# Kernel optimization log

Hardware: AMD Instinct MI355X
Metric: run time of the kernel (lower is better)

## Reference

```python
import jax, jax.numpy as jnp
import numpy as np

N_NODES = 50000
N_EDGES = 1000000
N_EVAL = 100000
IN_DIM = 256
HID = 64
HEADS = 4
NEG_SLOPE = 0.2


def _glorot(key, shape):
    fan_in, fan_out = shape[0], shape[-1]
    lim = jnp.sqrt(6.0 / (fan_in + fan_out))
    return jax.random.uniform(key, shape, jnp.float32, -lim, lim)


def setup_inputs() -> dict:
    key = jax.random.key(0)
    ks = jax.random.split(key, 24)
    inp = {}
    inp["x"] = jax.random.normal(ks[0], (N_NODES, IN_DIM), jnp.float32)
    inp["edge_index"] = jax.random.randint(ks[1], (2, N_EDGES), 0, N_NODES, jnp.int64)
    inp["edge_src"] = jax.random.randint(ks[2], (N_EVAL,), 0, N_NODES, jnp.int64)
    inp["edge_dst"] = jax.random.randint(ks[3], (N_EVAL,), 0, N_NODES, jnp.int64)
    # encoder
    inp["enc_w"] = _glorot(ks[4], (IN_DIM, HID))
    inp["enc_b"] = jnp.zeros((HID,), jnp.float32)
    # GAT layer 1: HID -> HEADS*HID (concat)
    inp["gat1_w"] = _glorot(ks[5], (HID, HEADS * HID))
    inp["gat1_att_src"] = _glorot(ks[6], (HEADS, HID))
    inp["gat1_att_dst"] = _glorot(ks[7], (HEADS, HID))
    inp["gat1_b"] = jnp.zeros((HEADS * HID,), jnp.float32)
    # GAT layer 2: HEADS*HID -> HEADS*HID
    inp["gat2_w"] = _glorot(ks[8], (HEADS * HID, HEADS * HID))
    inp["gat2_att_src"] = _glorot(ks[9], (HEADS, HID))
    inp["gat2_att_dst"] = _glorot(ks[10], (HEADS, HID))
    inp["gat2_b"] = jnp.zeros((HEADS * HID,), jnp.float32)
    # link predictor MLP: 2*256 -> 64 -> 32 -> 1
    inp["lp1_w"] = _glorot(ks[11], (2 * HEADS * HID, HID))
    inp["lp1_b"] = jnp.zeros((HID,), jnp.float32)
    inp["lp2_w"] = _glorot(ks[12], (HID, HID // 2))
    inp["lp2_b"] = jnp.zeros((HID // 2,), jnp.float32)
    inp["lp3_w"] = _glorot(ks[13], (HID // 2, 1))
    inp["lp3_b"] = jnp.zeros((1,), jnp.float32)
    return inp


def gat_layer(x, src, dst, W, att_src, att_dst, bias, n_nodes):
    # x: [N, F_in] -> h: [N, H, C]
    h = (x @ W).reshape(n_nodes, HEADS, HID)
    a_s = jnp.einsum("nhc,hc->nh", h, att_src)  # per-node src logit part
    a_d = jnp.einsum("nhc,hc->nh", h, att_dst)  # per-node dst logit part
    e = jax.nn.leaky_relu(a_s[src] + a_d[dst], NEG_SLOPE)  # [E, H]
    # segment softmax over incoming edges of each dst node
    m = jax.ops.segment_max(e, dst, num_segments=n_nodes)  # [N, H]
    e = jnp.exp(e - m[dst])
    s = jax.ops.segment_sum(e, dst, num_segments=n_nodes)  # [N, H]
    alpha = e / (s[dst] + 1e-16)  # [E, H]
    msg = h[src] * alpha[:, :, None]  # [E, H, C]
    out = jax.ops.segment_sum(msg, dst, num_segments=n_nodes)  # [N, H, C]
    return out.reshape(n_nodes, HEADS * HID) + bias


def reference(x, edge_index, edge_src, edge_dst,
              enc_w, enc_b,
              gat1_w, gat1_att_src, gat1_att_dst, gat1_b,
              gat2_w, gat2_att_src, gat2_att_dst, gat2_b,
              lp1_w, lp1_b, lp2_w, lp2_b, lp3_w, lp3_b):
    n = x.shape[0]
    src, dst = edge_index[0], edge_index[1]
    # NodeEncoder
    h = jax.nn.relu(x @ enc_w + enc_b)
    # GAT layers (dropout is identity in eval)
    h = gat_layer(h, src, dst, gat1_w, gat1_att_src, gat1_att_dst, gat1_b, n)
    h = gat_layer(h, src, dst, gat2_w, gat2_att_src, gat2_att_dst, gat2_b, n)
    # link predictor on (src_feat, dst_feat) pairs
    pair = jnp.concatenate([h[edge_src], h[edge_dst]], axis=1)  # [Eval, 512]
    z = jax.nn.relu(pair @ lp1_w + lp1_b)
    z = jax.nn.relu(z @ lp2_w + lp2_b)
    scores = z @ lp3_w + lp3_b  # [Eval, 1]
    return scores
```

## Files before the change

kernel.cpp:

```cpp
#include <hip/hip_runtime.h>
#include <hip/hip_bf16.h>
#include <math.h>

#define NNODES 50000
#define HID    64
#define HEADS  4
#define FDIM   256

typedef __attribute__((ext_vector_type(8))) _Float16 half8v;
typedef __attribute__((ext_vector_type(4))) _Float16 half4v;
typedef __attribute__((ext_vector_type(4))) float f32x4;

__device__ __forceinline__ float lrelu(float x) { return fmaxf(x, 0.2f * x); }

__global__ void prep_kernel(const float4* __restrict__ x, _Float16* __restrict__ xh, int n4,
                            const float* __restrict__ enc_w, const float* __restrict__ g1_w,
                            const float* __restrict__ g2_w, const float* __restrict__ lp1_w,
                            const float* __restrict__ g1_as, const float* __restrict__ g1_ad,
                            const float* __restrict__ g2_as, const float* __restrict__ g2_ad,
                            _Float16* __restrict__ we, _Float16* __restrict__ w1,
                            _Float16* __restrict__ w2, _Float16* __restrict__ wlp)
{
  int t = blockIdx.x * blockDim.x + threadIdx.x;
  if (t < n4) {
    float4 v = x[t];
    half4v o = {(_Float16)v.x, (_Float16)v.y, (_Float16)v.z, (_Float16)v.w};
    *(half4v*)(xh + (size_t)t * 4) = o;
    return;
  }
  int u = t - n4;
  if (u < 16384) {
    int n = u >> 8, k = u & 255;
    we[u] = (_Float16)enc_w[(size_t)k * 64 + n];
  } else if (u < 32768) {
    int l = u - 16384; int n = l >> 6, k = l & 63;
    w1[l] = (_Float16)g1_w[(size_t)k * 256 + n];
  } else if (u < 98304) {
    int l = u - 32768; int n = l >> 8, k = l & 255;
    w2[l] = (_Float16)g2_w[(size_t)k * 256 + n];
  } else if (u < 131072) {
    int l = u - 98304; int n = l >> 8, k = l & 255;
    int srow = (n < 64) ? k : (256 + k);
    wlp[l] = (_Float16)lp1_w[(size_t)srow * 64 + (n & 63)];
  } else if (u < 132096) {
    int l = u - 131072; int j = l >> 6, k = l & 63;
    float v = 0.f;
    if (j < 8) {
      int head = j & 3;
      const float* att = (j < 4 ? g1_as : g1_ad) + head * 64;
      for (int c = 0; c < 64; ++c) v += g1_w[(size_t)k * 256 + head * 64 + c] * att[c];
    }
    w1[(256 + j) * 64 + k] = (_Float16)v;
  } else if (u < 136192) {
    int l = u - 132096; int j = l >> 8, k = l & 255;
    float v = 0.f;
    if (j < 8) {
      int head = j & 3;
      const float* att = (j < 4 ? g2_as : g2_ad) + head * 64;
      for (int c = 0; c < 64; ++c) v += g2_w[(size_t)k * 256 + head * 64 + c] * att[c];
    }
    w2[(256 + j) * 256 + k] = (_Float16)v;
  }
}

__global__ __launch_bounds__(256) void enc_gemm(
    const _Float16* __restrict__ A, const _Float16* __restrict__ B,
    const float* __restrict__ bias, _Float16* __restrict__ outH, int M)
{
  __shared__ _Float16 As[128 * 64];
  const int tid  = threadIdx.x;
  const int lane = tid & 63;
  const int wid  = tid >> 6;
  const int row0 = blockIdx.y * 128;

  f32x4 acc[2][4];
#pragma unroll
  for (int m = 0; m < 2; ++m)
#pragma unroll
    for (int n = 0; n < 4; ++n) acc[m][n] = (f32x4){0.f, 0.f, 0.f, 0.f};

  const int rsub = lane >> 3;
  const int slot = lane & 7;
  const int brow = lane & 15;
  const int bk   = (lane >> 4) * 8;

  for (int kt = 0; kt < 256; kt += 64) {
#pragma unroll
    for (int i = 0; i < 4; ++i) {
      const int c  = i * 4 + wid;
      const int r  = c * 8 + rsub;
      const int gr = min(row0 + r, M - 1);
      const int ss = slot ^ rsub;
      const size_t goff = (size_t)gr * 256 + kt + ss * 8;
      __builtin_amdgcn_global_load_lds(
          (const __attribute__((address_space(1))) void*)(A + goff),
          (__attribute__((address_space(3))) void*)(As + c * 512), 16, 0, 0);
    }
    __syncthreads();

#pragma unroll
    for (int ks = 0; ks < 2; ++ks) {
      half8v ah[2], bh[4];
#pragma unroll
      for (int mf = 0; mf < 2; ++mf) {
        const int r   = wid * 32 + mf * 16 + (lane & 15);
        const int sl  = (ks * 4 + (lane >> 4)) ^ (r & 7);
        ah[mf] = *(const half8v*)(As + r * 64 + sl * 8);
      }
#pragma unroll
      for (int nf = 0; nf < 4; ++nf)
        bh[nf] = *(const half8v*)(B + (size_t)(brow + nf * 16) * 256 + kt + ks * 32 + bk);
#pragma unroll
      for (int mf = 0; mf < 2; ++mf)
#pragma unroll
        for (int nf = 0; nf < 4; ++nf)
          acc[mf][nf] = __builtin_amdgcn_mfma_f32_16x16x32_f16(ah[mf], bh[nf], acc[mf][nf], 0, 0, 0);
    }
    __syncthreads();
  }

  const int crow = row0 + wid * 32 + (lane >> 4) * 4;
  const int ccol = lane & 15;
#pragma unroll
  for (int mf = 0; mf < 2; ++mf)
#pragma unroll
    for (int nf = 0; nf < 4; ++nf)
#pragma unroll
      for (int r = 0; r < 4; ++r) {
        const int grow = crow + mf * 16 + r;
        const int gcol = ccol + nf * 16;
        if (grow >= M) continue;
        float v = fmaxf(acc[mf][nf][r] + bias[gcol], 0.f);
        outH[(size_t)grow * HID + gcol] = (_Float16)v;
      }
}

template<int KTOT, bool LOGIT>
__global__ __launch_bounds__(512) void gemm512(
    const _Float16* __restrict__ A, const _Float16* __restrict__ B,
    _Float16* __restrict__ outH, float* __restrict__ a_s, float* __restrict__ a_d,
    int M, int OS)
{
  __shared__ _Float16 As[128 * KTOT];
  constexpr int SPR = KTOT / 8;
  const int tid  = threadIdx.x;
  const int lane = tid & 63;
  const int w    = tid >> 6;
  const int rowg = w & 3;
  const int colg = w >> 2;
  const int row0 = blockIdx.y * 128;
  const int col0 = blockIdx.x * 128 + colg * 64;
  const bool lastlog = LOGIT && ((int)blockIdx.x == (int)gridDim.x - 1) && (colg == 1);

#pragma unroll
  for (int rr = 0; rr < KTOT / 32; ++rr) {
    const int f  = rr * 512 + tid;
    const int r  = f / SPR;
    const int s  = f % SPR;
    const int gs = s ^ (r & 7);
    const int gr = min(row0 + r, M - 1);
    __builtin_amdgcn_global_load_lds(
        (const __attribute__((address_space(1))) void*)(A + (size_t)gr * KTOT + gs * 8),
        (__attribute__((address_space(3))) void*)(As + f * 8), 16, 0, 0);
  }
  __syncthreads();

  f32x4 acc[2][4];
  f32x4 accL[2];
#pragma unroll
  for (int m = 0; m < 2; ++m) {
#pragma unroll
    for (int n = 0; n < 4; ++n) acc[m][n] = (f32x4){0.f, 0.f, 0.f, 0.f};
    accL[m] = (f32x4){0.f, 0.f, 0.f, 0.f};
  }

  const int brow = col0 + (lane & 15);
#pragma unroll
  for (int ks = 0; ks < KTOT / 32; ++ks) {
    const int sk = ks * 4 + (lane >> 4);
    half8v ah[2];
#pragma unroll
    for (int mf = 0; mf < 2; ++mf) {
      const int r = rowg * 32 + mf * 16 + (lane & 15);
      ah[mf] = *(const half8v*)(As + r * KTOT + (sk ^ (r & 7)) * 8);
    }
#pragma unroll
    for (int nf = 0; nf < 4; ++nf) {
      const half8v bh = *(const half8v*)(B + (size_t)(brow + nf * 16) * KTOT + sk * 8);
      acc[0][nf] = __builtin_amdgcn_mfma_f32_16x16x32_f16(ah[0], bh, acc[0][nf], 0, 0, 0);
      acc[1][nf] = __builtin_amdgcn_mfma_f32_16x16x32_f16(ah[1], bh, acc[1][nf], 0, 0, 0);
    }
    if (lastlog) {
      const half8v bh = *(const half8v*)(B + (size_t)(256 + (lane & 15)) * KTOT + sk * 8);
      accL[0] = __builtin_amdgcn_mfma_f32_16x16x32_f16(ah[0], bh, accL[0], 0, 0, 0);
      accL[1] = __builtin_amdgcn_mfma_f32_16x16x32_f16(ah[1], bh, accL[1], 0, 0, 0);
    }
  }

  const int crow = row0 + rowg * 32 + (lane >> 4) * 4;
  const int ccol = col0 + (lane & 15);
#pragma unroll
  for (int mf = 0; mf < 2; ++mf)
#pragma unroll
    for (int nf = 0; nf < 4; ++nf)
#pragma unroll
      for (int r = 0; r < 4; ++r) {
        const int grow = crow + mf * 16 + r;
        if (grow >= M) continue;
        outH[(size_t)grow * OS + ccol + nf * 16] = (_Float16)acc[mf][nf][r];
      }
  if (lastlog) {
    const int c8 = lane & 15;
#pragma unroll
    for (int mf = 0; mf < 2; ++mf)
#pragma unroll
      for (int r = 0; r < 4; ++r) {
        const int grow = crow + mf * 16 + r;
        if (grow >= M) continue;
        const float v = accL[mf][r];
        if (c8 < 4)      a_s[grow * 4 + c8] = v;
        else if (c8 < 8) a_d[grow * 4 + (c8 - 4)] = v;
      }
  }
}

__global__ void hist_kernel(const int* __restrict__ dst, int* __restrict__ deg, int E)
{
  int i = blockIdx.x * blockDim.x + threadIdx.x;
  if (i < E) atomicAdd(&deg[dst[i]], 1);
}

__global__ void scan1_kernel(const int* __restrict__ deg, int* __restrict__ off,
                             int* __restrict__ bsum, int n)
{
  __shared__ int ws[4];
  const int t = threadIdx.x, lane = t & 63, w = t >> 6;
  const int i = blockIdx.x * 256 + t;
  const int v = (i < n) ? deg[i] : 0;
  int x = v;
#pragma unroll
  for (int d = 1; d < 64; d <<= 1) {
    int y = __shfl_up(x, d, 64);
    if (lane >= d) x += y;
  }
  if (lane == 63) ws[w] = x;
  __syncthreads();
  int add = 0;
  for (int k = 0; k < w; ++k) add += ws[k];
  if (i < n) off[i] = add + x - v;
  if (t == 255) bsum[blockIdx.x] = add + x;
}

__global__ void scan2_kernel(int* __restrict__ bsum, int nb)
{
  __shared__ int ws[4];
  const int t = threadIdx.x, lane = t & 63, w = t >> 6;
  const int v = (t < nb) ? bsum[t] : 0;
  int x = v;
#pragma unroll
  for (int d = 1; d < 64; d <<= 1) {
    int y = __shfl_up(x, d, 64);
    if (lane >= d) x += y;
  }
  if (lane == 63) ws[w] = x;
  __syncthreads();
  int add = 0;
  for (int k = 0; k < w; ++k) add += ws[k];
  if (t < nb) bsum[t] = add + x - v;
}

__global__ void scan3_kernel(int* __restrict__ off, const int* __restrict__ bsum, int n, int E)
{
  const int i = blockIdx.x * 256 + threadIdx.x;
  if (i < n) off[i] += bsum[blockIdx.x];
  if (i == 0) off[n] = E;
}

__global__ void scatter_kernel(const int* __restrict__ src, const int* __restrict__ dst,
                               const int* __restrict__ off, int* __restrict__ cursor,
                               int* __restrict__ sidx, int E)
{
  int i = blockIdx.x * blockDim.x + threadIdx.x;
  if (i < E) {
    int d = dst[i];
    int p = atomicAdd(&cursor[d], 1);
    sidx[off[d] + p] = src[i];
  }
}

__global__ __launch_bounds__(256) void aggregate_kernel(
    const _Float16* __restrict__ hW, const int* __restrict__ sidx,
    const int* __restrict__ off, const float* __restrict__ a_s, const float* __restrict__ a_d,
    const float* __restrict__ bias,
    _Float16* __restrict__ outH, int n_nodes)
{
  __shared__ float wlds[4][16][4];
  const int w    = threadIdx.x >> 6;
  const int wid  = (blockIdx.x * 256 + threadIdx.x) >> 6;
  const int lane = threadIdx.x & 63;
  if (wid >= n_nodes) return;
  const int n = wid;
  const int beg = off[n], end = off[n + 1];

  const int es   = lane >> 2;
  const int hh   = lane & 3;
  const float adh = a_d[(unsigned)n * 4 + hh];
  float m = -1e30f, ssum = 0.f;
  for (int j = beg + es; j < end; j += 16) {
    const unsigned s = (unsigned)sidx[j];
    const float e = lrelu(a_s[s * 4 + hh] + adh);
    const float mn = fmaxf(m, e);
    ssum = ssum * __expf(m - mn) + __expf(e - mn);
    m = mn;
  }
#pragma unroll
  for (int d = 4; d < 64; d <<= 1) {
    const float mo = __shfl_xor(m, d, 64);
    const float so = __shfl_xor(ssum, d, 64);
    const float mn = fmaxf(m, mo);
    ssum = ssum * __expf(m - mn) + so * __expf(mo - mn);
    m = mn;
  }
  const int hb = lane >> 4;
  const float sh = __shfl(ssum, hb, 64);

  float acc0 = 0.f, acc1 = 0.f, acc2 = 0.f, acc3 = 0.f;
  const unsigned lo4 = (unsigned)(lane << 2);
  for (int j0 = beg; j0 < end; j0 += 16) {
    const int jj = j0 + es;
    float wv = 0.f;
    if (jj < end) {
      const unsigned s = (unsigned)sidx[jj];
      const float e = lrelu(a_s[s * 4 + hh] + adh);
      wv = __expf(e - m);
    }
    wlds[w][es][hh] = wv;
    const int jend = min(j0 + 16, end);
#pragma unroll 4
    for (int j = j0; j < jend; ++j) {
      const unsigned s = (unsigned)sidx[j];
      const float wgt = wlds[w][j - j0][hb];
      const half4v hv = *(const half4v*)(hW + s * (unsigned)FDIM + lo4);
      acc0 = fmaf(wgt, (float)hv.x, acc0);
      acc1 = fmaf(wgt, (float)hv.y, acc1);
      acc2 = fmaf(wgt, (float)hv.z, acc2);
      acc3 = fmaf(wgt, (float)hv.w, acc3);
    }
  }
  const float inv = 1.f / (sh + 1e-16f);
  const float4 bv = *(const float4*)(bias + lo4);
  half4v o = {(_Float16)(acc0 * inv + bv.x), (_Float16)(acc1 * inv + bv.y),
              (_Float16)(acc2 * inv + bv.z), (_Float16)(acc3 * inv + bv.w)};
  *(half4v*)(outH + (unsigned)n * FDIM + lo4) = o;
}

__global__ __launch_bounds__(256) void linkpred_kernel(
    const _Float16* __restrict__ uv,
    const int* __restrict__ es, const int* __restrict__ ed,
    const float* __restrict__ b1, const float* __restrict__ w2, const float* __restrict__ b2,
    const float* __restrict__ w3, const float* __restrict__ b3,
    float* __restrict__ out, int n_eval)
{
  __shared__ float w2s[64 * 32];
  __shared__ float z1s[4][4][64];
  const int t = threadIdx.x;
  for (int i = t; i < 64 * 32; i += 256) w2s[i] = w2[i];
  const int w = t >> 6, lane = t & 63;
  const int pair0 = blockIdx.x * 16 + w * 4;
#pragma unroll
  for (int p = 0; p < 4; ++p) {
    const int pc = min(pair0 + p, n_eval - 1);
    const int s = es[pc], d = ed[pc];
    const float uvl = (float)uv[(unsigned)s * 128 + lane] + (float)uv[(unsigned)d * 128 + 64 + lane];
    z1s[w][p][lane] = fmaxf(uvl + b1[lane], 0.f);
  }
  __syncthreads();
  const int half = lane >> 5;
  const int col  = lane & 31;
  const float w3c = w3[col];
#pragma unroll
  for (int pp = 0; pp < 2; ++pp) {
    const int p = pp * 2 + half;
    float acc = b2[col];
#pragma unroll
    for (int k = 0; k < 64; ++k) acc = fmaf(z1s[w][p][k], w2s[k * 32 + col], acc);
    float zz = fmaxf(acc, 0.f) * w3c;
#pragma unroll
    for (int d = 1; d < 32; d <<= 1) zz += __shfl_xor(zz, d, 64);
    if (col == 0) {
      const int pv = pair0 + p;
      if (pv < n_eval) out[pv] = zz + b3[0];
    }
  }
}

extern "C" void kernel_launch(void* const* d_in, const int* in_sizes, int n_in,
                              void* d_out, int out_size, void* d_ws, size_t ws_size,
                              hipStream_t stream)
{
  const float* x     = (const float*)d_in[0];
  const int*   ei    = (const int*)d_in[1];
  const int*   esrc  = (const int*)d_in[2];
  const int*   edst  = (const int*)d_in[3];
  const float* enc_w = (const float*)d_in[4];
  const float* enc_b = (const float*)d_in[5];
  const float* g1_w  = (const float*)d_in[6];
  const float* g1_as = (const float*)d_in[7];
  const float* g1_ad = (const float*)d_in[8];
  const float* g1_b  = (const float*)d_in[9];
  const float* g2_w  = (const float*)d_in[10];
  const float* g2_as = (const float*)d_in[11];
  const float* g2_ad = (const float*)d_in[12];
  const float* g2_b  = (const float*)d_in[13];
  const float* lp1_w = (const float*)d_in[14];
  const float* lp1_b = (const float*)d_in[15];
  const float* lp2_w = (const float*)d_in[16];
  const float* lp2_b = (const float*)d_in[17];
  const float* lp3_w = (const float*)d_in[18];
  const float* lp3_b = (const float*)d_in[19];
  float* out = (float*)d_out;

  const int E  = in_sizes[1] / 2;
  const int NE = in_sizes[2];
  const int M  = NNODES;
  const int NB = (M + 255) / 256;

  const int* e_src = ei;
  const int* e_dst = ei + E;

  _Float16* hWh = (_Float16*)d_ws;
  float* a_s   = (float*)(hWh + (size_t)M * FDIM);
  float* a_d   = a_s + (size_t)M * HEADS;
  _Float16* hh = (_Float16*)(a_d + (size_t)M * HEADS);
  _Float16* agg = hh + (size_t)M * HID;
  int*   deg    = (int*)(agg + (size_t)M * FDIM);
  int*   cursor = deg + M;
  int*   off    = cursor + M;
  int*   bsum   = off + M + 1;
  int*   sidx   = bsum + 256;
  _Float16* we  = (_Float16*)(sidx + E);
  _Float16* w1  = we + 64 * 256;
  _Float16* w2  = w1 + 272 * 64;
  _Float16* wlp = w2 + 272 * 256;
  _Float16* x_h = agg;
  _Float16* uv = hWh;

  hipMemsetAsync(deg, 0, sizeof(int) * 2 * (size_t)M, stream);
  hist_kernel<<<(E + 255) / 256, 256, 0, stream>>>(e_dst, deg, E);
  scan1_kernel<<<NB, 256, 0, stream>>>(deg, off, bsum, M);
  scan2_kernel<<<1, 256, 0, stream>>>(bsum, NB);
  scan3_kernel<<<NB, 256, 0, stream>>>(off, bsum, M, E);
  scatter_kernel<<<(E + 255) / 256, 256, 0, stream>>>(e_src, e_dst, off, cursor, sidx, E);

  {
    const int n4 = M * FDIM / 4;
    const int total = n4 + 136192;
    prep_kernel<<<(total + 255) / 256, 256, 0, stream>>>(
        (const float4*)x, x_h, n4, enc_w, g1_w, g2_w, lp1_w,
        g1_as, g1_ad, g2_as, g2_ad, we, w1, w2, wlp);
  }

  const int GB = (M + 127) / 128;

  enc_gemm<<<dim3(1, GB), 256, 0, stream>>>(x_h, we, enc_b, hh, M);

  gemm512<64, true><<<dim3(2, GB), 512, 0, stream>>>(hh, w1, hWh, a_s, a_d, M, FDIM);
  aggregate_kernel<<<(M * 64 + 255) / 256, 256, 0, stream>>>(
      hWh, sidx, off, a_s, a_d, g1_b, agg, M);

  gemm512<256, true><<<dim3(2, GB), 512, 0, stream>>>(agg, w2, hWh, a_s, a_d, M, FDIM);
  aggregate_kernel<<<(M * 64 + 255) / 256, 256, 0, stream>>>(
      hWh, sidx, off, a_s, a_d, g2_b, agg, M);

  gemm512<256, false><<<dim3(1, GB), 512, 0, stream>>>(agg, wlp, uv, nullptr, nullptr, M, 2 * HID);
  linkpred_kernel<<<(NE + 15) / 16, 256, 0, stream>>>(uv, esrc, edst, lp1_b, lp2_w, lp2_b,
                                                      lp3_w, lp3_b, out, NE);
}
```

Baseline: 517.6 us.

## Fuse encoder into GAT1 GEMM, use global max for softmax, drop scan3/hist kernels

Folds the degree histogram into the prep kernel and removes the scan3 pass by adding block sums at use sites. Fuses the encoder GEMM with the first GAT projection so the hidden features stay in LDS. Replaces the per-node online softmax max pass in aggregation with a global per-head upper bound, built from atomicMax over encoded floats, which removes one pass over the edges. The global max shift risks underflow for nodes whose logits sit far below the bound, and the encoder work is now repeated by both column blocks.

After: 734.0 us. +41.8%, slower.

```diff
diff --git a/kernel.cpp b/kernel.cpp
--- a/kernel.cpp
+++ b/kernel.cpp
@@ -12,6 +12,14 @@
 typedef __attribute__((ext_vector_type(4))) float f32x4;
 
 __device__ __forceinline__ float lrelu(float x) { return fmaxf(x, 0.2f * x); }
+
+__device__ __forceinline__ unsigned fenc(float f) {
+  unsigned u = __float_as_uint(f);
+  return (u & 0x80000000u) ? ~u : (u | 0x80000000u);
+}
+__device__ __forceinline__ float fdec(unsigned u) {
+  return (u & 0x80000000u) ? __uint_as_float(u & 0x7fffffffu) : __uint_as_float(~u);
+}
 
 __global__ void prep_kernel(const float4* __restrict__ x, _Float16* __restrict__ xh, int n4,
                             const float* __restrict__ enc_w, const float* __restrict__ g1_w,
@@ -19,7 +27,8 @@
                             const float* __restrict__ g1_as, const float* __restrict__ g1_ad,
                             const float* __restrict__ g2_as, const float* __restrict__ g2_ad,
                             _Float16* __restrict__ we, _Float16* __restrict__ w1,
-                            _Float16* __restrict__ w2, _Float16* __restrict__ wlp)
+                            _Float16* __restrict__ w2, _Float16* __restrict__ wlp,
+                            const int* __restrict__ e_dst, int* __restrict__ deg, int E)
 {
   int t = blockIdx.x * blockDim.x + threadIdx.x;
   if (t < n4) {
@@ -60,67 +69,110 @@
       for (int c = 0; c < 64; ++c) v += g2_w[(size_t)k * 256 + head * 64 + c] * att[c];
     }
     w2[(256 + j) * 256 + k] = (_Float16)v;
-  }
-}
-
-__global__ __launch_bounds__(256) void enc_gemm(
-    const _Float16* __restrict__ A, const _Float16* __restrict__ B,
-    const float* __restrict__ bias, _Float16* __restrict__ outH, int M)
-{
-  __shared__ _Float16 As[128 * 64];
+  } else {
+    int i = u - 136192;
+    if (i < E) atomicAdd(&deg[e_dst[i]], 1);
+  }
+}
+
+__global__ __launch_bounds__(512) void encg1_gemm(
+    const _Float16* __restrict__ X, const _Float16* __restrict__ We,
+    const float* __restrict__ encb, const _Float16* __restrict__ W1,
+    _Float16* __restrict__ outH, float* __restrict__ a_s, float* __restrict__ a_d,
+    unsigned* __restrict__ ms, int M)
+{
+  __shared__ _Float16 Xs[128 * 64];
+  __shared__ _Float16 Hs[128 * 64];
   const int tid  = threadIdx.x;
   const int lane = tid & 63;
-  const int wid  = tid >> 6;
+  const int w    = tid >> 6;
   const int row0 = blockIdx.y * 128;
 
+  f32x4 acc1[4];
+#pragma unroll
+  for (int n = 0; n < 4; ++n) acc1[n] = (f32x4){0.f, 0.f, 0.f, 0.f};
+
+  for (int kt = 0; kt < 256; kt += 64) {
+#pragma unroll
+    for (int i = 0; i < 2; ++i) {
+      const int f  = i * 512 + tid;
+      const int r  = f >> 3;
+      const int s  = f & 7;
+      const int gs = s ^ (r & 7);
+      const int gr = min(row0 + r, M - 1);
+      __builtin_amdgcn_global_load_lds(
+          (const __attribute__((address_space(1))) void*)(X + (size_t)gr * 256 + kt + gs * 8),
+          (__attribute__((address_space(3))) void*)(Xs + f * 8), 16, 0, 0);
+    }
+    __syncthreads();
+#pragma unroll
+    for (int ks = 0; ks < 2; ++ks) {
+      const int r  = w * 16 + (lane & 15);
+      const int sk = ks * 4 + (lane >> 4);
+      const half8v ah = *(const half8v*)(Xs + r * 64 + (sk ^ (r & 7)) * 8);
+#pragma unroll
+      for (int nf = 0; nf < 4; ++nf) {
+        const int c = (lane & 15) + nf * 16;
+        const half8v bh = *(const half8v*)(We + (size_t)c * 256 + kt + ks * 32 + (lane >> 4) * 8);
+        acc1[nf] = __builtin_amdgcn_mfma_f32_16x16x32_f16(ah, bh, acc1[nf], 0, 0, 0);
+      }
+    }
+    __syncthreads();
+  }
+  {
+    const int lr0 = w * 16 + (lane >> 4) * 4;
+#pragma unroll
+    for (int nf = 0; nf < 4; ++nf) {
+      const int c = (lane & 15) + nf * 16;
+      const float b = encb[c];
+#pragma unroll
+      for (int r = 0; r < 4; ++r) {
+        const int lr = lr0 + r;
+        const float v = fmaxf(acc1[nf][r] + b, 0.f);
+        Hs[lr * 64 + ((c >> 3) ^ (lr & 7)) * 8 + (c & 7)] = (_Float16)v;
+      }
+    }
+  }
+  __syncthreads();
+
+  const int rowg = w & 3;
+  const int colg = w >> 2;
+  const int col0 = blockIdx.x * 128 + colg * 64;
+  const bool lastlog = ((int)blockIdx.x == 1) && (colg == 1);
+
   f32x4 acc[2][4];
-#pragma unroll
-  for (int m = 0; m < 2; ++m)
+  f32x4 accL[2];
+#pragma unroll
+  for (int m = 0; m < 2; ++m) {
 #pragma unroll
     for (int n = 0; n < 4; ++n) acc[m][n] = (f32x4){0.f, 0.f, 0.f, 0.f};
-
-  const int rsub = lane >> 3;
-  const int slot = lane & 7;
-  const int brow = lane & 15;
-  const int bk   = (lane >> 4) * 8;
-
-  for (int kt = 0; kt < 256; kt += 64) {
-#pragma unroll
-    for (int i = 0; i < 4; ++i) {
-      const int c  = i * 4 + wid;
-      const int r  = c * 8 + rsub;
-      const int gr = min(row0 + r, M - 1);
-      const int ss = slot ^ rsub;
-      const size_t goff = (size_t)gr * 256 + kt + ss * 8;
-      __builtin_amdgcn_global_load_lds(
-          (const __attribute__((address_space(1))) void*)(A + goff),
-          (__attribute__((address_space(3))) void*)(As + c * 512), 16, 0, 0);
-    }
-    __syncthreads();
-
-#pragma unroll
-    for (int ks = 0; ks < 2; ++ks) {
-      half8v ah[2], bh[4];
-#pragma unroll
-      for (int mf = 0; mf < 2; ++mf) {
-        const int r   = wid * 32 + mf * 16 + (lane & 15);
-        const int sl  = (ks * 4 + (lane >> 4)) ^ (r & 7);
-        ah[mf] = *(const half8v*)(As + r * 64 + sl * 8);
-      }
-#pragma unroll
-      for (int nf = 0; nf < 4; ++nf)
-        bh[nf] = *(const half8v*)(B + (size_t)(brow + nf * 16) * 256 + kt + ks * 32 + bk);
-#pragma unroll
-      for (int mf = 0; mf < 2; ++mf)
-#pragma unroll
-        for (int nf = 0; nf < 4; ++nf)
-          acc[mf][nf] = __builtin_amdgcn_mfma_f32_16x16x32_f16(ah[mf], bh[nf], acc[mf][nf], 0, 0, 0);
-    }
-    __syncthreads();
-  }
-
-  const int crow = row0 + wid * 32 + (lane >> 4) * 4;
-  const int ccol = lane & 15;
+    accL[m] = (f32x4){0.f, 0.f, 0.f, 0.f};
+  }
+  const int brow = col0 + (lane & 15);
+#pragma unroll
+  for (int ks = 0; ks < 2; ++ks) {
+    const int sk = ks * 4 + (lane >> 4);
+    half8v ah[2];
+#pragma unroll
+    for (int mf = 0; mf < 2; ++mf) {
+      const int r = rowg * 32 + mf * 16 + (lane & 15);
+      ah[mf] = *(const half8v*)(Hs + r * 64 + (sk ^ (r & 7)) * 8);
+    }
+#pragma unroll
+    for (int nf = 0; nf < 4; ++nf) {
+      const half8v bh = *(const half8v*)(W1 + (size_t)(brow + nf * 16) * 64 + sk * 8);
+      acc[0][nf] = __builtin_amdgcn_mfma_f32_16x16x32_f16(ah[0], bh, acc[0][nf], 0, 0, 0);
+      acc[1][nf] = __builtin_amdgcn_mfma_f32_16x16x32_f16(ah[1], bh, acc[1][nf], 0, 0, 0);
+    }
+    if (lastlog) {
+      const half8v bh = *(const half8v*)(W1 + (size_t)(256 + (lane & 15)) * 64 + sk * 8);
+      accL[0] = __builtin_amdgcn_mfma_f32_16x16x32_f16(ah[0], bh, accL[0], 0, 0, 0);
+      accL[1] = __builtin_amdgcn_mfma_f32_16x16x32_f16(ah[1], bh, accL[1], 0, 0, 0);
+    }
+  }
+
+  const int crow = row0 + rowg * 32 + (lane >> 4) * 4;
+  const int ccol = col0 + (lane & 15);
 #pragma unroll
   for (int mf = 0; mf < 2; ++mf)
 #pragma unroll
@@ -128,18 +180,32 @@
 #pragma unroll
       for (int r = 0; r < 4; ++r) {
         const int grow = crow + mf * 16 + r;
-        const int gcol = ccol + nf * 16;
         if (grow >= M) continue;
-        float v = fmaxf(acc[mf][nf][r] + bias[gcol], 0.f);
-        outH[(size_t)grow * HID + gcol] = (_Float16)v;
+        outH[(size_t)grow * FDIM + ccol + nf * 16] = (_Float16)acc[mf][nf][r];
       }
+  if (lastlog) {
+    const int c8 = lane & 15;
+    float vmax = -1e30f;
+#pragma unroll
+    for (int mf = 0; mf < 2; ++mf)
+#pragma unroll
+      for (int r = 0; r < 4; ++r) {
+        const int grow = crow + mf * 16 + r;
+        const float v = accL[mf][r];
+        vmax = fmaxf(vmax, v);
+        if (grow >= M) continue;
+        if (c8 < 4)      a_s[grow * 4 + c8] = v;
+        else if (c8 < 8) a_d[grow * 4 + (c8 - 4)] = v;
+      }
+    if (c8 < 8) atomicMax(&ms[c8], fenc(vmax));
+  }
 }
 
 template<int KTOT, bool LOGIT>
 __global__ __launch_bounds__(512) void gemm512(
     const _Float16* __restrict__ A, const _Float16* __restrict__ B,
     _Float16* __restrict__ outH, float* __restrict__ a_s, float* __restrict__ a_d,
-    int M, int OS)
+    unsigned* __restrict__ ms, int M, int OS)
 {
   __shared__ _Float16 As[128 * KTOT];
   constexpr int SPR = KTOT / 8;
@@ -211,23 +277,20 @@
       }
   if (lastlog) {
     const int c8 = lane & 15;
+    float vmax = -1e30f;
 #pragma unroll
     for (int mf = 0; mf < 2; ++mf)
 #pragma unroll
       for (int r = 0; r < 4; ++r) {
         const int grow = crow + mf * 16 + r;
+        const float v = accL[mf][r];
+        vmax = fmaxf(vmax, v);
         if (grow >= M) continue;
-        const float v = accL[mf][r];
         if (c8 < 4)      a_s[grow * 4 + c8] = v;
         else if (c8 < 8) a_d[grow * 4 + (c8 - 4)] = v;
       }
-  }
-}
-
-__global__ void hist_kernel(const int* __restrict__ dst, int* __restrict__ deg, int E)
-{
-  int i = blockIdx.x * blockDim.x + threadIdx.x;
-  if (i < E) atomicAdd(&deg[dst[i]], 1);
+    if (c8 < 8) atomicMax(&ms[c8], fenc(vmax));
+  }
 }
 
 __global__ void scan1_kernel(const int* __restrict__ deg, int* __restrict__ off,
@@ -269,29 +332,23 @@
   if (t < nb) bsum[t] = add + x - v;
 }
 
-__global__ void scan3_kernel(int* __restrict__ off, const int* __restrict__ bsum, int n, int E)
-{
-  const int i = blockIdx.x * 256 + threadIdx.x;
-  if (i < n) off[i] += bsum[blockIdx.x];
-  if (i == 0) off[n] = E;
-}
-
 __global__ void scatter_kernel(const int* __restrict__ src, const int* __restrict__ dst,
-                               const int* __restrict__ off, int* __restrict__ cursor,
-                               int* __restrict__ sidx, int E)
+                               const int* __restrict__ off, const int* __restrict__ bsum,
+                               int* __restrict__ cursor, int* __restrict__ sidx, int E)
 {
   int i = blockIdx.x * blockDim.x + threadIdx.x;
   if (i < E) {
     int d = dst[i];
     int p = atomicAdd(&cursor[d], 1);
-    sidx[off[d] + p] = src[i];
+    sidx[off[d] + bsum[d >> 8] + p] = src[i];
   }
 }
 
 __global__ __launch_bounds__(256) void aggregate_kernel(
     const _Float16* __restrict__ hW, const int* __restrict__ sidx,
-    const int* __restrict__ off, const float* __restrict__ a_s, const float* __restrict__ a_d,
-    const float* __restrict__ bias,
+    const int* __restrict__ off, const int* __restrict__ bsum, const int* __restrict__ deg,
+    const float* __restrict__ a_s, const float* __restrict__ a_d,
+    const unsigned* __restrict__ ms, const float* __restrict__ bias,
     _Float16* __restrict__ outH, int n_nodes)
 {
   __shared__ float wlds[4][16][4];
@@ -300,30 +357,16 @@
   const int lane = threadIdx.x & 63;
   if (wid >= n_nodes) return;
   const int n = wid;
-  const int beg = off[n], end = off[n + 1];
-
-  const int es   = lane >> 2;
-  const int hh   = lane & 3;
+  const int beg = off[n] + bsum[n >> 8];
+  const int end = beg + deg[n];
+
+  const int es = lane >> 2;
+  const int hh = lane & 3;
+  const float Mh  = lrelu(fdec(ms[hh]) + fdec(ms[4 + hh]));
   const float adh = a_d[(unsigned)n * 4 + hh];
-  float m = -1e30f, ssum = 0.f;
-  for (int j = beg + es; j < end; j += 16) {
-    const unsigned s = (unsigned)sidx[j];
-    const float e = lrelu(a_s[s * 4 + hh] + adh);
-    const float mn = fmaxf(m, e);
-    ssum = ssum * __expf(m - mn) + __expf(e - mn);
-    m = mn;
-  }
-#pragma unroll
-  for (int d = 4; d < 64; d <<= 1) {
-    const float mo = __shfl_xor(m, d, 64);
-    const float so = __shfl_xor(ssum, d, 64);
-    const float mn = fmaxf(m, mo);
-    ssum = ssum * __expf(m - mn) + so * __expf(mo - mn);
-    m = mn;
-  }
   const int hb = lane >> 4;
-  const float sh = __shfl(ssum, hb, 64);
-
+
+  float ssum = 0.f;
   float acc0 = 0.f, acc1 = 0.f, acc2 = 0.f, acc3 = 0.f;
   const unsigned lo4 = (unsigned)(lane << 2);
   for (int j0 = beg; j0 < end; j0 += 16) {
@@ -331,10 +374,10 @@
     float wv = 0.f;
     if (jj < end) {
       const unsigned s = (unsigned)sidx[jj];
-      const float e = lrelu(a_s[s * 4 + hh] + adh);
-      wv = __expf(e - m);
+      wv = __expf(lrelu(a_s[s * 4 + hh] + adh) - Mh);
     }
     wlds[w][es][hh] = wv;
+    ssum += wv;
     const int jend = min(j0 + 16, end);
 #pragma unroll 4
     for (int j = j0; j < jend; ++j) {
@@ -347,6 +390,10 @@
       acc3 = fmaf(wgt, (float)hv.w, acc3);
     }
   }
+#pragma unroll
+  for (int d = 4; d < 64; d <<= 1) ssum += __shfl_xor(ssum, d, 64);
+  const float sh = __shfl(ssum, hb, 64);
+
   const float inv = 1.f / (sh + 1e-16f);
   const float4 bv = *(const float4*)(bias + lo4);
   half4v o = {(_Float16)(acc0 * inv + bv.x), (_Float16)(acc1 * inv + bv.y),
@@ -431,11 +478,11 @@
   _Float16* hWh = (_Float16*)d_ws;
   float* a_s   = (float*)(hWh + (size_t)M * FDIM);
   float* a_d   = a_s + (size_t)M * HEADS;
-  _Float16* hh = (_Float16*)(a_d + (size_t)M * HEADS);
-  _Float16* agg = hh + (size_t)M * HID;
+  _Float16* agg = (_Float16*)(a_d + (size_t)M * HEADS);
   int*   deg    = (int*)(agg + (size_t)M * FDIM);
   int*   cursor = deg + M;
-  int*   off    = cursor + M;
+  unsigned* ms  = (unsigned*)(cursor + M);
+  int*   off    = (int*)(ms + 16);
   int*   bsum   = off + M + 1;
   int*   sidx   = bsum + 256;
   _Float16* we  = (_Float16*)(sidx + E);
@@ -445,34 +492,31 @@
   _Float16* x_h = agg;
   _Float16* uv = hWh;
 
-  hipMemsetAsync(deg, 0, sizeof(int) * 2 * (size_t)M, stream);
-  hist_kernel<<<(E + 255) / 256, 256, 0, stream>>>(e_dst, deg, E);
+  hipMemsetAsync(deg, 0, sizeof(int) * (2 * (size_t)M + 16), stream);
+
+  {
+    const int n4 = M * FDIM / 4;
+    const int total = n4 + 136192 + E;
+    prep_kernel<<<(total + 255) / 256, 256, 0, stream>>>(
+        (const float4*)x, x_h, n4, enc_w, g1_w, g2_w, lp1_w,
+        g1_as, g1_ad, g2_as, g2_ad, we, w1, w2, wlp, e_dst, deg, E);
+  }
+
   scan1_kernel<<<NB, 256, 0, stream>>>(deg, off, bsum, M);
   scan2_kernel<<<1, 256, 0, stream>>>(bsum, NB);
-  scan3_kernel<<<NB, 256, 0, stream>>>(off, bsum, M, E);
-  scatter_kernel<<<(E + 255) / 256, 256, 0, stream>>>(e_src, e_dst, off, cursor, sidx, E);
-
-  {
-    const int n4 = M * FDIM / 4;
-    const int total = n4 + 136192;
-    prep_kernel<<<(total + 255) / 256, 256, 0, stream>>>(
-        (const float4*)x, x_h, n4, enc_w, g1_w, g2_w, lp1_w,
-        g1_as, g1_ad, g2_as, g2_ad, we, w1, w2, wlp);
-  }
+  scatter_kernel<<<(E + 255) / 256, 256, 0, stream>>>(e_src, e_dst, off, bsum, cursor, sidx, E);
 
   const int GB = (M + 127) / 128;
 
-  enc_gemm<<<dim3(1, GB), 256, 0, stream>>>(x_h, we, enc_b, hh, M);
-
-  gemm512<64, true><<<dim3(2, GB), 512, 0, stream>>>(hh, w1, hWh, a_s, a_d, M, FDIM);
+  encg1_gemm<<<dim3(2, GB), 512, 0, stream>>>(x_h, we, enc_b, w1, hWh, a_s, a_d, ms, M);
   aggregate_kernel<<<(M * 64 + 255) / 256, 256, 0, stream>>>(
-      hWh, sidx, off, a_s, a_d, g1_b, agg, M);
-
-  gemm512<256, true><<<dim3(2, GB), 512, 0, stream>>>(agg, w2, hWh, a_s, a_d, M, FDIM);
+      hWh, sidx, off, bsum, deg, a_s, a_d, ms, g1_b, agg, M);
+
+  gemm512<256, true><<<dim3(2, GB), 512, 0, stream>>>(agg, w2, hWh, a_s, a_d, ms + 8, M, FDIM);
   aggregate_kernel<<<(M * 64 + 255) / 256, 256, 0, stream>>>(
-      hWh, sidx, off, a_s, a_d, g2_b, agg, M);
-
-  gemm512<256, false><<<dim3(1, GB), 512, 0, stream>>>(agg, wlp, uv, nullptr, nullptr, M, 2 * HID);
+      hWh, sidx, off, bsum, deg, a_s, a_d, ms + 8, g2_b, agg, M);
+
+  gemm512<256, false><<<dim3(1, GB), 512, 0, stream>>>(agg, wlp, uv, nullptr, nullptr, nullptr, M, 2 * HID);
   linkpred_kernel<<<(NE + 15) / 16, 256, 0, stream>>>(uv, esrc, edst, lp1_b, lp2_w, lp2_b,
                                                       lp3_w, lp3_b, out, NE);
 }
```
